# Optimization experiments

Measured on AMD Instinct MI355X. Metric: run time of the kernel, lower is better.

## Reference

```python
import jax, jax.numpy as jnp
import numpy as np

EPS = 1e-6
ROPE_BASE = 10000.0


def layer_norm(x, scale, bias):
    mu = jnp.mean(x, axis=-1, keepdims=True)
    var = jnp.mean(jnp.square(x - mu), axis=-1, keepdims=True)
    return (x - mu) * jax.lax.rsqrt(var + EPS) * scale + bias


def make_rope(head_dim, seq_len):
    half = head_dim // 2
    inv_freq = 1.0 / (ROPE_BASE ** (jnp.arange(half, dtype=jnp.float32) / half))
    freqs = jnp.outer(jnp.arange(seq_len, dtype=jnp.float32), inv_freq)  # (T, half)
    cos = jnp.concatenate([jnp.cos(freqs), jnp.cos(freqs)], axis=-1)[:, None, :]  # (T,1,Dh)
    sin = jnp.concatenate([jnp.sin(freqs), jnp.sin(freqs)], axis=-1)[:, None, :]

    def rotate_half(x):
        x1, x2 = x[..., :half], x[..., half:]
        return jnp.concatenate([-x2, x1], axis=-1)

    def apply(q, k):
        return q * cos + rotate_half(q) * sin, k * cos + rotate_half(k) * sin
    return apply


def mha(x, Wq, bq, Wk, bk, Wv, bv, Wo, bo, causal, rope):
    # x: (..., S, D) -> (..., S, D)
    q = jnp.einsum('...sd,dhk->...shk', x, Wq) + bq
    k = jnp.einsum('...sd,dhk->...shk', x, Wk) + bk
    v = jnp.einsum('...sd,dhk->...shk', x, Wv) + bv
    if rope is not None:
        q, k = rope(q, k)
    scale = 1.0 / np.sqrt(q.shape[-1]).astype(np.float32)
    logits = jnp.einsum('...thk,...shk->...hts', q, k) * scale
    if causal:
        S = q.shape[-3]
        mask = jnp.tril(jnp.ones((S, S), dtype=jnp.bool_))
        logits = jnp.where(mask, logits, jnp.finfo(logits.dtype).min)
    probs = jax.nn.softmax(logits, axis=-1)
    o = jnp.einsum('...hts,...shk->...thk', probs, v)
    return jnp.einsum('...thk,hkd->...td', o, Wo) + bo


def setup_inputs() -> dict:
    key = jax.random.key(0)
    B, T, M, D, H, Dh, F = 8, 128, 16, 1024, 16, 64, 4096
    ks = jax.random.split(key, 12)
    s = 0.02
    return {
        'x': jax.random.normal(ks[0], (B, T, M, D), jnp.float32),
        'ln1_scale': jnp.ones((D,), jnp.float32), 'ln1_bias': jnp.zeros((D,), jnp.float32),
        't_Wq': jax.random.normal(ks[1], (D, H, Dh), jnp.float32) * s,
        't_bq': jnp.zeros((H, Dh), jnp.float32),
        't_Wk': jax.random.normal(ks[2], (D, H, Dh), jnp.float32) * s,
        't_bk': jnp.zeros((H, Dh), jnp.float32),
        't_Wv': jax.random.normal(ks[3], (D, H, Dh), jnp.float32) * s,
        't_bv': jnp.zeros((H, Dh), jnp.float32),
        't_Wo': jax.random.normal(ks[4], (H, Dh, D), jnp.float32) * s,
        't_bo': jnp.zeros((D,), jnp.float32),
        'ln2_scale': jnp.ones((D,), jnp.float32), 'ln2_bias': jnp.zeros((D,), jnp.float32),
        'm_Wq': jax.random.normal(ks[5], (D, H, Dh), jnp.float32) * s,
        'm_bq': jnp.zeros((H, Dh), jnp.float32),
        'm_Wk': jax.random.normal(ks[6], (D, H, Dh), jnp.float32) * s,
        'm_bk': jnp.zeros((H, Dh), jnp.float32),
        'm_Wv': jax.random.normal(ks[7], (D, H, Dh), jnp.float32) * s,
        'm_bv': jnp.zeros((H, Dh), jnp.float32),
        'm_Wo': jax.random.normal(ks[8], (H, Dh, D), jnp.float32) * s,
        'm_bo': jnp.zeros((D,), jnp.float32),
        'ln3_scale': jnp.ones((D,), jnp.float32), 'ln3_bias': jnp.zeros((D,), jnp.float32),
        'mlp_W1': jax.random.normal(ks[9], (D, F), jnp.float32) * s,
        'mlp_b1': jnp.zeros((F,), jnp.float32),
        'mlp_W2': jax.random.normal(ks[10], (F, D), jnp.float32) * s,
        'mlp_b2': jnp.zeros((D,), jnp.float32),
    }


def reference(x, ln1_scale, ln1_bias, t_Wq, t_bq, t_Wk, t_bk, t_Wv, t_bv, t_Wo, t_bo,
              ln2_scale, ln2_bias, m_Wq, m_bq, m_Wk, m_bk, m_Wv, m_bv, m_Wo, m_bo,
              ln3_scale, ln3_bias, mlp_W1, mlp_b1, mlp_W2, mlp_b2):
    # x: (B, T, M, D)
    T = x.shape[1]
    Dh = t_Wq.shape[-1]
    rope = make_rope(Dh, T)
    # --- temporal axial attention (causal, RoPE), M folded into batch ---
    h = layer_norm(x, ln1_scale, ln1_bias)
    h = jnp.swapaxes(h, 1, 2)  # (B, M, T, D)
    a = mha(h, t_Wq, t_bq, t_Wk, t_bk, t_Wv, t_bv, t_Wo, t_bo, causal=True, rope=rope)
    x = x + jnp.swapaxes(a, 1, 2)
    # --- modality axial attention (bidirectional, no RoPE), T folded into batch ---
    h = layer_norm(x, ln2_scale, ln2_bias)  # (B, T, M, D), M is seq axis
    x = x + mha(h, m_Wq, m_bq, m_Wk, m_bk, m_Wv, m_bv, m_Wo, m_bo, causal=False, rope=None)
    # --- MLP ---
    h = layer_norm(x, ln3_scale, ln3_bias)
    h = jax.nn.gelu(jnp.einsum('...d,df->...f', h, mlp_W1) + mlp_b1)
    x = x + jnp.einsum('...f,fd->...d', h, mlp_W2) + mlp_b2
    return x
```

## Files before the change

kernel.cpp:

```cpp
#include <hip/hip_runtime.h>
#include <stdint.h>

typedef __attribute__((ext_vector_type(8))) __bf16 bf16x8;
typedef __attribute__((ext_vector_type(4))) float f32x4;

#define DEV static __device__ __forceinline__

DEV unsigned short f2bf(float f) {
    unsigned int u = __float_as_uint(f);
    u = (u + 0x7fffu + ((u >> 16) & 1u)) >> 16;
    return (unsigned short)u;
}
DEV float bf2f(unsigned short h) { return __uint_as_float((unsigned int)h << 16); }

DEV void async_ld16(const void* g, void* l) {
    __builtin_amdgcn_global_load_lds(
        (const __attribute__((address_space(1))) void*)g,
        (__attribute__((address_space(3))) void*)l, 16, 0, 0);
}

DEV f32x4 mfma16(bf16x8 a, bf16x8 b, f32x4 c) {
    return __builtin_amdgcn_mfma_f32_16x16x32_bf16(a, b, c, 0, 0, 0);
}

DEV float gelu_f(float v) {
    float u = 0.7978845608028654f * (v + 0.044715f * v * v * v);
    u = fminf(fmaxf(u, -9.f), 9.f);
    const float e = __expf(2.f * u);
    const float th = (e - 1.f) / (e + 1.f);
    return 0.5f * v * (1.0f + th);
}

__global__ __launch_bounds__(256) void wconv_kernel(
    const float* __restrict__ src, unsigned short* __restrict__ dst, int K, int N)
{
    __shared__ float tile[32][33];
    const int tx = threadIdx.x & 31;
    const int ty = threadIdx.x >> 5;
    const long nb = blockIdx.x;
    const long kb = blockIdx.y;
#pragma unroll
    for (int i = 0; i < 32; i += 8)
        tile[ty + i][tx] = src[(kb * 32 + ty + i) * N + nb * 32 + tx];
    __syncthreads();
#pragma unroll
    for (int i = 0; i < 32; i += 8)
        dst[(nb * 32 + ty + i) * K + kb * 32 + tx] = f2bf(tile[tx][ty + i]);
}

__global__ void pack_bias_kernel(const float* __restrict__ bq, const float* __restrict__ bk,
                                 const float* __restrict__ bv, float* __restrict__ o)
{
    int i = blockIdx.x * 256 + threadIdx.x;
    if (i < 1024) o[i] = bq[i];
    else if (i < 2048) o[i] = bk[i - 1024];
    else if (i < 3072) o[i] = bv[i - 2048];
}

__global__ __launch_bounds__(256) void ln_kernel(
    const float* __restrict__ x, const float* __restrict__ scale,
    const float* __restrict__ bias, unsigned short* __restrict__ out)
{
    const int lane = threadIdx.x & 63;
    const int wave = threadIdx.x >> 6;
    const long tok = (long)blockIdx.x * 4 + wave;
    const float* xp = x + tok * 1024;
    float4 v[4];
    float sum = 0.f, sq = 0.f;
#pragma unroll
    for (int i = 0; i < 4; ++i) {
        v[i] = ((const float4*)xp)[i * 64 + lane];
        sum += v[i].x + v[i].y + v[i].z + v[i].w;
        sq += v[i].x * v[i].x + v[i].y * v[i].y + v[i].z * v[i].z + v[i].w * v[i].w;
    }
#pragma unroll
    for (int off = 1; off < 64; off <<= 1) {
        sum += __shfl_xor(sum, off);
        sq  += __shfl_xor(sq, off);
    }
    const float mu = sum * (1.f / 1024.f);
    const float var = sq * (1.f / 1024.f) - mu * mu;
    const float rs = rsqrtf(var + 1e-6f);
#pragma unroll
    for (int i = 0; i < 4; ++i) {
        const float4 sc = ((const float4*)scale)[i * 64 + lane];
        const float4 bi = ((const float4*)bias)[i * 64 + lane];
        ushort4 o;
        o.x = f2bf((v[i].x - mu) * rs * sc.x + bi.x);
        o.y = f2bf((v[i].y - mu) * rs * sc.y + bi.y);
        o.z = f2bf((v[i].z - mu) * rs * sc.z + bi.z);
        o.w = f2bf((v[i].w - mu) * rs * sc.w + bi.w);
        *(ushort4*)&out[tok * 1024 + (i * 64 + lane) * 4] = o;
    }
}

template <int EPI, bool ROPE>
__global__ __launch_bounds__(256, 3) void gemm128_kernel(
    const unsigned short* __restrict__ A, const unsigned short* __restrict__ Bt,
    const float* __restrict__ bias, const float* __restrict__ resid,
    void* __restrict__ Cout, int M, int N, int K, int nbx)
{
    __shared__ __align__(16) unsigned short lds[2][2][4096];
    const int tid = threadIdx.x;
    const int lane = tid & 63;
    const int wave = tid >> 6;
    const int wr = wave >> 1;
    const int wc = wave & 1;
    const int lr = lane & 15;
    const int hi = lane >> 4;

    const int nwg = gridDim.x;
    const int cpx = nwg >> 3;
    int bid = blockIdx.x;
    bid = (bid & 7) * cpx + (bid >> 3);
    const int bx = bid % nbx, by = bid / nbx;
    const long row0 = (long)by * 128;
    const long col0 = (long)bx * 128;
    const int NT = K >> 5;

    const int r_ = tid >> 2;
    const int pc = tid & 3;
    const int sxr = (r_ >> 1) & 3;
    const unsigned short* gA0 = A + (row0 + r_) * (long)K + (pc ^ sxr) * 8;
    const unsigned short* gA1 = A + (row0 + r_ + 64) * (long)K + (pc ^ sxr) * 8;
    const unsigned short* gB0 = Bt + (col0 + r_) * (long)K + (pc ^ sxr) * 8;
    const unsigned short* gB1 = Bt + (col0 + r_ + 64) * (long)K + (pc ^ sxr) * 8;

    auto stage = [&](int buf, int kt) {
        const long ko = (long)kt * 32;
        async_ld16(gA0 + ko, &lds[buf][0][tid * 8]);
        async_ld16(gA1 + ko, &lds[buf][0][tid * 8 + 2048]);
        async_ld16(gB0 + ko, &lds[buf][1][tid * 8]);
        async_ld16(gB1 + ko, &lds[buf][1][tid * 8 + 2048]);
    };

    int aoff[4], boff[4];
#pragma unroll
    for (int m = 0; m < 4; ++m) {
        const int row = wr * 64 + m * 16 + lr;
        aoff[m] = row * 64 + ((hi ^ ((row >> 1) & 3)) << 4);
    }
#pragma unroll
    for (int n = 0; n < 4; ++n) {
        const int row = wc * 64 + n * 16 + lr;
        boff[n] = row * 64 + ((hi ^ ((row >> 1) & 3)) << 4);
    }

    f32x4 acc[4][4];
#pragma unroll
    for (int i = 0; i < 4; ++i)
#pragma unroll
        for (int j = 0; j < 4; ++j) acc[i][j] = f32x4{0.f, 0.f, 0.f, 0.f};

    stage(0, 0);

    for (int kt = 0; kt < NT; ++kt) {
        const int b = kt & 1;
        if (kt + 1 < NT) stage(b ^ 1, kt + 1);
        __builtin_amdgcn_sched_barrier(0);
        if (kt + 1 < NT) { asm volatile("s_waitcnt vmcnt(4)" ::: "memory"); }
        else             { asm volatile("s_waitcnt vmcnt(0)" ::: "memory"); }
        __builtin_amdgcn_sched_barrier(0);
        __builtin_amdgcn_s_barrier();
        __builtin_amdgcn_sched_barrier(0);

        const char* bA = (const char*)&lds[b][0][0];
        const char* bB = (const char*)&lds[b][1][0];
        bf16x8 a[4], bf[4];
#pragma unroll
        for (int n = 0; n < 4; ++n) bf[n] = *(const bf16x8*)(bB + boff[n]);
#pragma unroll
        for (int m = 0; m < 4; ++m) a[m] = *(const bf16x8*)(bA + aoff[m]);

        __builtin_amdgcn_s_setprio(1);
#pragma unroll
        for (int m = 0; m < 4; ++m)
#pragma unroll
            for (int n = 0; n < 4; ++n)
                acc[m][n] = mfma16(a[m], bf[n], acc[m][n]);
        __builtin_amdgcn_s_setprio(0);

        __builtin_amdgcn_sched_barrier(0);
        __builtin_amdgcn_s_barrier();
        __builtin_amdgcn_sched_barrier(0);
    }

    __syncthreads();

    float bcol[4];
#pragma unroll
    for (int n = 0; n < 4; ++n) bcol[n] = bias[col0 + wc * 64 + n * 16 + lr];

    if (EPI == 2) {
        float (*eF)[128] = (float (*)[128])&lds[0][0][0];
        float* co = (float*)Cout;
#pragma unroll
        for (int half = 0; half < 2; ++half) {
            if (wr == half) {
#pragma unroll
                for (int m = 0; m < 4; ++m)
#pragma unroll
                    for (int n = 0; n < 4; ++n)
#pragma unroll
                        for (int j = 0; j < 4; ++j)
                            eF[m * 16 + hi * 4 + j][wc * 64 + n * 16 + lr] =
                                acc[m][n][j] + bcol[n];
            }
            __syncthreads();
#pragma unroll
            for (int it = 0; it < 8; ++it) {
                const int idx = it * 256 + tid;
                const int row = idx >> 5;
                const int ch = (idx & 31) * 4;
                const long g = row0 + half * 64 + row;
                float4 v = *(const float4*)&eF[row][ch];
                const float4 rv = *(const float4*)&resid[g * N + col0 + ch];
                v.x += rv.x; v.y += rv.y; v.z += rv.z; v.w += rv.w;
                *(float4*)&co[g * N + col0 + ch] = v;
            }
            __syncthreads();
        }
    } else {
        unsigned short (*eT)[128] = (unsigned short (*)[128])&lds[0][0][0];
        unsigned short* co = (unsigned short*)Cout;
        const bool doRope = ROPE && (col0 + wc * 64) < 2048;
        if (doRope) {
#pragma unroll
            for (int m = 0; m < 4; ++m) {
                const float t_i = (float)(int)(((row0 + wr * 64 + m * 16) >> 4) & 127);
#pragma unroll
                for (int n = 0; n < 2; ++n) {
                    const float dd = (float)(n * 16 + lr);
                    const float inv = __expf(dd * -0.2878231366242557f);
                    float sn, cs;
                    __sincosf(t_i * inv, &sn, &cs);
#pragma unroll
                    for (int j = 0; j < 4; ++j) {
                        const float lo = acc[m][n][j] + bcol[n];
                        const float hv = acc[m][n + 2][j] + bcol[n + 2];
                        eT[wr * 64 + m * 16 + hi * 4 + j][wc * 64 + n * 16 + lr] = f2bf(lo * cs - hv * sn);
                        eT[wr * 64 + m * 16 + hi * 4 + j][wc * 64 + 32 + n * 16 + lr] = f2bf(hv * cs + lo * sn);
                    }
                }
            }
        } else {
#pragma unroll
            for (int m = 0; m < 4; ++m)
#pragma unroll
                for (int n = 0; n < 4; ++n)
#pragma unroll
                    for (int j = 0; j < 4; ++j) {
                        float v = acc[m][n][j] + bcol[n];
                        if (EPI == 1) v = gelu_f(v);
                        eT[wr * 64 + m * 16 + hi * 4 + j][wc * 64 + n * 16 + lr] = f2bf(v);
                    }
        }
        __syncthreads();
#pragma unroll
        for (int it = 0; it < 8; ++it) {
            const int idx = it * 256 + tid;
            const int row = idx >> 4;
            const int ch = (idx & 15) * 8;
            *(uint4*)&co[(row0 + row) * N + col0 + ch] = *(const uint4*)&eT[row][ch];
        }
    }
}

__global__ __launch_bounds__(256) void attn_temporal(
    const unsigned short* __restrict__ qkv, unsigned short* __restrict__ out)
{
    const int bid = blockIdx.x;
    const int h = bid & 15;
    const int mm = (bid >> 4) & 15;
    const int b = bid >> 8;
    const int tid = threadIdx.x;
    const int lane = tid & 63;
    const int wave = tid >> 6;
    const int lr = lane & 15;
    const int lk = (lane >> 4) * 8;
    const int r4 = (lane >> 4) * 4;

    __shared__ __align__(16) unsigned short smemA[128 * 136];
    __shared__ __align__(16) unsigned short smemV[64 * 136];
    unsigned short (*Ks)[72] = (unsigned short (*)[72])smemA;
    unsigned short (*Ps)[136] = (unsigned short (*)[136])smemA;
    unsigned short (*Vt)[136] = (unsigned short (*)[136])smemV;

    const long tokbase = (long)b * 2048 + mm;

#pragma unroll
    for (int i = 0; i < 4; ++i) {
        const int cc = tid + 256 * i;
        const int s = cc >> 3, part = cc & 7;
        const unsigned short* g = qkv + (tokbase + s * 16l) * 3072 + 1024 + h * 64 + part * 8;
        *(uint4*)&Ks[s][part * 8] = *(const uint4*)g;
    }
#pragma unroll
    for (int i = 0; i < 4; ++i) {
        const int cc = tid + 256 * i;
        const int s = cc >> 3, part = cc & 7;
        const unsigned short* g = qkv + (tokbase + s * 16l) * 3072 + 2048 + h * 64 + part * 8;
        union { uint4 u; unsigned short us[8]; } uu;
        uu.u = *(const uint4*)g;
#pragma unroll
        for (int j = 0; j < 8; ++j) Vt[part * 8 + j][s] = uu.us[j];
    }
    __syncthreads();

    bf16x8 qf[2][2];
#pragma unroll
    for (int rb = 0; rb < 2; ++rb)
#pragma unroll
        for (int ks = 0; ks < 2; ++ks) {
            const int t = wave * 32 + rb * 16 + lr;
            qf[rb][ks] = *(const bf16x8*)(qkv + (tokbase + t * 16l) * 3072 + h * 64 + ks * 32 + lk);
        }

    f32x4 sacc[2][8];
#pragma unroll
    for (int rb = 0; rb < 2; ++rb)
#pragma unroll
        for (int cb = 0; cb < 8; ++cb) sacc[rb][cb] = f32x4{0.f, 0.f, 0.f, 0.f};

#pragma unroll
    for (int cb = 0; cb < 8; ++cb)
#pragma unroll
        for (int ks = 0; ks < 2; ++ks) {
            const bf16x8 kf = *(const bf16x8*)&Ks[cb * 16 + lr][ks * 32 + lk];
            sacc[0][cb] = mfma16(qf[0][ks], kf, sacc[0][cb]);
            sacc[1][cb] = mfma16(qf[1][ks], kf, sacc[1][cb]);
        }

    float recip[2][4];
#pragma unroll
    for (int rb = 0; rb < 2; ++rb)
#pragma unroll
        for (int r = 0; r < 4; ++r) {
            const int trow = wave * 32 + rb * 16 + r4 + r;
            float mx = -1e30f;
#pragma unroll
            for (int cb = 0; cb < 8; ++cb) {
                const int s = cb * 16 + lr;
                const float v = (s <= trow) ? sacc[rb][cb][r] * 0.125f : -1e30f;
                sacc[rb][cb][r] = v;
                mx = fmaxf(mx, v);
            }
            mx = fmaxf(mx, __shfl_xor(mx, 1));
            mx = fmaxf(mx, __shfl_xor(mx, 2));
            mx = fmaxf(mx, __shfl_xor(mx, 4));
            mx = fmaxf(mx, __shfl_xor(mx, 8));
            float sum = 0.f;
#pragma unroll
            for (int cb = 0; cb < 8; ++cb) {
                const float e = __expf(sacc[rb][cb][r] - mx);
                sacc[rb][cb][r] = e;
                sum += e;
            }
            sum += __shfl_xor(sum, 1);
            sum += __shfl_xor(sum, 2);
            sum += __shfl_xor(sum, 4);
            sum += __shfl_xor(sum, 8);
            recip[rb][r] = 1.f / sum;
        }
    __syncthreads();

#pragma unroll
    for (int rb = 0; rb < 2; ++rb)
#pragma unroll
        for (int cb = 0; cb < 8; ++cb)
#pragma unroll
            for (int r = 0; r < 4; ++r)
                Ps[wave * 32 + rb * 16 + r4 + r][cb * 16 + lr] = f2bf(sacc[rb][cb][r]);
    __syncthreads();

    f32x4 oacc[2][4];
#pragma unroll
    for (int rb = 0; rb < 2; ++rb)
#pragma unroll
        for (int cb = 0; cb < 4; ++cb) oacc[rb][cb] = f32x4{0.f, 0.f, 0.f, 0.f};

#pragma unroll
    for (int ks = 0; ks < 4; ++ks) {
        bf16x8 pf[2];
        pf[0] = *(const bf16x8*)&Ps[wave * 32 + lr][ks * 32 + lk];
        pf[1] = *(const bf16x8*)&Ps[wave * 32 + 16 + lr][ks * 32 + lk];
#pragma unroll
        for (int cb = 0; cb < 4; ++cb) {
            const bf16x8 vf = *(const bf16x8*)&Vt[cb * 16 + lr][ks * 32 + lk];
            oacc[0][cb] = mfma16(pf[0], vf, oacc[0][cb]);
            oacc[1][cb] = mfma16(pf[1], vf, oacc[1][cb]);
        }
    }

#pragma unroll
    for (int rb = 0; rb < 2; ++rb)
#pragma unroll
        for (int cb = 0; cb < 4; ++cb)
#pragma unroll
            for (int r = 0; r < 4; ++r) {
                const int trow = wave * 32 + rb * 16 + r4 + r;
                out[(tokbase + trow * 16l) * 1024 + h * 64 + cb * 16 + lr] =
                    f2bf(oacc[rb][cb][r] * recip[rb][r]);
            }
}

__global__ __launch_bounds__(256) void attn_modality(
    const unsigned short* __restrict__ qkv, unsigned short* __restrict__ out)
{
    const int tid = threadIdx.x;
    const int lane = tid & 63;
    const int wave = tid >> 6;
    const int lr = lane & 15;
    const int lk = (lane >> 4) * 8;
    const int r4 = (lane >> 4) * 4;
    const long base = (long)blockIdx.x * 16;

    __shared__ __align__(16) unsigned short smem[4][64 * 40 + 16 * 40];
    unsigned short (*Vt)[40] = (unsigned short (*)[40]) & smem[wave][0];
    unsigned short (*Pl)[40] = (unsigned short (*)[40]) & smem[wave][64 * 40];

    for (int i = lane; i < 400; i += 64)
        *(uint4*)&smem[wave][i * 8] = make_uint4(0u, 0u, 0u, 0u);

    for (int hi = 0; hi < 4; ++hi) {
        const int h = wave * 4 + hi;
#pragma unroll
        for (int i = 0; i < 2; ++i) {
            const int cc = lane + 64 * i;
            const int s = cc >> 3, d0 = (cc & 7) * 8;
            union { uint4 u; unsigned short us[8]; } uu;
            uu.u = *(const uint4*)(qkv + (base + s) * 3072 + 2048 + h * 64 + d0);
#pragma unroll
            for (int j = 0; j < 8; ++j) Vt[d0 + j][s] = uu.us[j];
        }
        bf16x8 qf[2], kf[2];
#pragma unroll
        for (int ks = 0; ks < 2; ++ks) {
            qf[ks] = *(const bf16x8*)(qkv + (base + lr) * 3072 + h * 64 + ks * 32 + lk);
            kf[ks] = *(const bf16x8*)(qkv + (base + lr) * 3072 + 1024 + h * 64 + ks * 32 + lk);
        }
        f32x4 sv = f32x4{0.f, 0.f, 0.f, 0.f};
        sv = mfma16(qf[0], kf[0], sv);
        sv = mfma16(qf[1], kf[1], sv);

        float recip[4], pe[4];
#pragma unroll
        for (int r = 0; r < 4; ++r) {
            const float v = sv[r] * 0.125f;
            float mx = v;
            mx = fmaxf(mx, __shfl_xor(mx, 1));
            mx = fmaxf(mx, __shfl_xor(mx, 2));
            mx = fmaxf(mx, __shfl_xor(mx, 4));
            mx = fmaxf(mx, __shfl_xor(mx, 8));
            const float e = __expf(v - mx);
            float sum = e;
            sum += __shfl_xor(sum, 1);
            sum += __shfl_xor(sum, 2);
            sum += __shfl_xor(sum, 4);
            sum += __shfl_xor(sum, 8);
            recip[r] = 1.f / sum;
            pe[r] = e;
        }
#pragma unroll
        for (int r = 0; r < 4; ++r) Pl[r4 + r][lr] = f2bf(pe[r]);

        const bf16x8 pf = *(const bf16x8*)&Pl[lr][lk];
#pragma unroll
        for (int cb = 0; cb < 4; ++cb) {
            const bf16x8 vf = *(const bf16x8*)&Vt[cb * 16 + lr][lk];
            f32x4 o = f32x4{0.f, 0.f, 0.f, 0.f};
            o = mfma16(pf, vf, o);
#pragma unroll
            for (int r = 0; r < 4; ++r)
                out[(base + r4 + r) * 1024 + h * 64 + cb * 16 + lr] = f2bf(o[r] * recip[r]);
        }
    }
}

extern "C" void kernel_launch(void* const* d_in, const int* in_sizes, int n_in,
                              void* d_out, int out_size, void* d_ws, size_t ws_size,
                              hipStream_t stream)
{
    (void)in_sizes; (void)n_in; (void)out_size;
    const float* x    = (const float*)d_in[0];
    const float* ln1s = (const float*)d_in[1];
    const float* ln1b = (const float*)d_in[2];
    const float* tWq  = (const float*)d_in[3];
    const float* tbq  = (const float*)d_in[4];
    const float* tWk  = (const float*)d_in[5];
    const float* tbk  = (const float*)d_in[6];
    const float* tWv  = (const float*)d_in[7];
    const float* tbv  = (const float*)d_in[8];
    const float* tWo  = (const float*)d_in[9];
    const float* tbo  = (const float*)d_in[10];
    const float* ln2s = (const float*)d_in[11];
    const float* ln2b = (const float*)d_in[12];
    const float* mWq  = (const float*)d_in[13];
    const float* mbq  = (const float*)d_in[14];
    const float* mWk  = (const float*)d_in[15];
    const float* mbk  = (const float*)d_in[16];
    const float* mWv  = (const float*)d_in[17];
    const float* mbv  = (const float*)d_in[18];
    const float* mWo  = (const float*)d_in[19];
    const float* mbo  = (const float*)d_in[20];
    const float* ln3s = (const float*)d_in[21];
    const float* ln3b = (const float*)d_in[22];
    const float* W1   = (const float*)d_in[23];
    const float* b1   = (const float*)d_in[24];
    const float* W2   = (const float*)d_in[25];
    const float* b2   = (const float*)d_in[26];

    if (ws_size < 201351168ull) return;

    char* ws = (char*)d_ws;
    unsigned short* Wt_tqkv = (unsigned short*)(ws + 0);
    unsigned short* Wt_to   = (unsigned short*)(ws + 6291456);
    unsigned short* Wt_mqkv = (unsigned short*)(ws + 8388608);
    unsigned short* Wt_mo   = (unsigned short*)(ws + 14680064);
    unsigned short* Wt1     = (unsigned short*)(ws + 16777216);
    unsigned short* Wt2     = (unsigned short*)(ws + 25165824);
    float* bias_t           = (float*)(ws + 33554432);
    float* bias_m           = (float*)(ws + 33566720);
    unsigned short* act     = (unsigned short*)(ws + 33579008);
    unsigned short* qkv     = (unsigned short*)(ws + 67133440);
    unsigned short* hidden  = qkv;
    float* xout = (float*)d_out;

    dim3 blk(256);

    wconv_kernel<<<dim3(32, 32), blk, 0, stream>>>(tWq, Wt_tqkv, 1024, 1024);
    wconv_kernel<<<dim3(32, 32), blk, 0, stream>>>(tWk, Wt_tqkv + 1024 * 1024, 1024, 1024);
    wconv_kernel<<<dim3(32, 32), blk, 0, stream>>>(tWv, Wt_tqkv + 2048 * 1024, 1024, 1024);
    wconv_kernel<<<dim3(32, 32), blk, 0, stream>>>(tWo, Wt_to, 1024, 1024);
    wconv_kernel<<<dim3(32, 32), blk, 0, stream>>>(mWq, Wt_mqkv, 1024, 1024);
    wconv_kernel<<<dim3(32, 32), blk, 0, stream>>>(mWk, Wt_mqkv + 1024 * 1024, 1024, 1024);
    wconv_kernel<<<dim3(32, 32), blk, 0, stream>>>(mWv, Wt_mqkv + 2048 * 1024, 1024, 1024);
    wconv_kernel<<<dim3(32, 32), blk, 0, stream>>>(mWo, Wt_mo, 1024, 1024);
    wconv_kernel<<<dim3(128, 32), blk, 0, stream>>>(W1, Wt1, 1024, 4096);
    wconv_kernel<<<dim3(32, 128), blk, 0, stream>>>(W2, Wt2, 4096, 1024);
    pack_bias_kernel<<<12, blk, 0, stream>>>(tbq, tbk, tbv, bias_t);
    pack_bias_kernel<<<12, blk, 0, stream>>>(mbq, mbk, mbv, bias_m);

    ln_kernel<<<4096, blk, 0, stream>>>(x, ln1s, ln1b, act);
    gemm128_kernel<0, true><<<3072, blk, 0, stream>>>(act, Wt_tqkv, bias_t, nullptr, qkv, 16384, 3072, 1024, 24);
    attn_temporal<<<2048, blk, 0, stream>>>(qkv, act);
    gemm128_kernel<2, false><<<1024, blk, 0, stream>>>(act, Wt_to, tbo, x, xout, 16384, 1024, 1024, 8);
    ln_kernel<<<4096, blk, 0, stream>>>(xout, ln2s, ln2b, act);
    gemm128_kernel<0, false><<<3072, blk, 0, stream>>>(act, Wt_mqkv, bias_m, nullptr, qkv, 16384, 3072, 1024, 24);
    attn_modality<<<1024, blk, 0, stream>>>(qkv, act);
    gemm128_kernel<2, false><<<1024, blk, 0, stream>>>(act, Wt_mo, mbo, xout, xout, 16384, 1024, 1024, 8);
    ln_kernel<<<4096, blk, 0, stream>>>(xout, ln3s, ln3b, act);
    gemm128_kernel<1, false><<<4096, blk, 0, stream>>>(act, Wt1, b1, nullptr, hidden, 16384, 4096, 1024, 32);
    gemm128_kernel<2, false><<<1024, blk, 0, stream>>>(hidden, Wt2, b2, xout, xout, 16384, 1024, 4096, 8);
}
```

Baseline: 861.1 us.

## Enlarge GEMM tile to 256x128 with 8-wave 512-thread blocks

Changes the GEMM from 128x128 tiles with 4 waves to 256x128 tiles with 8 waves (512 threads), so each B tile loaded into LDS is shared by twice as many rows. Global loads per k-step per thread drop from 4 to 3, and the epilogues are restaged in quarters or halves through the same LDS buffer. The goal is less global and LDS traffic for B per output element and fewer blocks. The cost is more epilogue barriers, a larger LDS footprint per block, and fewer blocks in the grid.

```diff
diff --git a/kernel.cpp b/kernel.cpp
--- a/kernel.cpp
+++ b/kernel.cpp
@@ -95,17 +95,17 @@
 }
 
 template <int EPI, bool ROPE>
-__global__ __launch_bounds__(256, 3) void gemm128_kernel(
+__global__ __launch_bounds__(512, 4) void gemm_kernel(
     const unsigned short* __restrict__ A, const unsigned short* __restrict__ Bt,
     const float* __restrict__ bias, const float* __restrict__ resid,
     void* __restrict__ Cout, int M, int N, int K, int nbx)
 {
-    __shared__ __align__(16) unsigned short lds[2][2][4096];
+    __shared__ __align__(16) unsigned short lds[2][12288];
     const int tid = threadIdx.x;
     const int lane = tid & 63;
     const int wave = tid >> 6;
-    const int wr = wave >> 1;
-    const int wc = wave & 1;
+    const int wm = wave >> 1;
+    const int wn = wave & 1;
     const int lr = lane & 15;
     const int hi = lane >> 4;
 
@@ -114,36 +114,33 @@
     int bid = blockIdx.x;
     bid = (bid & 7) * cpx + (bid >> 3);
     const int bx = bid % nbx, by = bid / nbx;
-    const long row0 = (long)by * 128;
+    const long row0 = (long)by * 256;
     const long col0 = (long)bx * 128;
     const int NT = K >> 5;
 
     const int r_ = tid >> 2;
-    const int pc = tid & 3;
-    const int sxr = (r_ >> 1) & 3;
-    const unsigned short* gA0 = A + (row0 + r_) * (long)K + (pc ^ sxr) * 8;
-    const unsigned short* gA1 = A + (row0 + r_ + 64) * (long)K + (pc ^ sxr) * 8;
-    const unsigned short* gB0 = Bt + (col0 + r_) * (long)K + (pc ^ sxr) * 8;
-    const unsigned short* gB1 = Bt + (col0 + r_ + 64) * (long)K + (pc ^ sxr) * 8;
+    const int gch = ((tid & 3) ^ ((tid >> 3) & 3)) * 8;
+    const unsigned short* srcA0 = A + (row0 + r_) * (long)K + gch;
+    const unsigned short* srcA1 = A + (row0 + 128 + r_) * (long)K + gch;
+    const unsigned short* srcB  = Bt + (col0 + r_) * (long)K + gch;
 
     auto stage = [&](int buf, int kt) {
         const long ko = (long)kt * 32;
-        async_ld16(gA0 + ko, &lds[buf][0][tid * 8]);
-        async_ld16(gA1 + ko, &lds[buf][0][tid * 8 + 2048]);
-        async_ld16(gB0 + ko, &lds[buf][1][tid * 8]);
-        async_ld16(gB1 + ko, &lds[buf][1][tid * 8 + 2048]);
+        async_ld16(srcA0 + ko, &lds[buf][tid * 8]);
+        async_ld16(srcA1 + ko, &lds[buf][4096 + tid * 8]);
+        async_ld16(srcB  + ko, &lds[buf][8192 + tid * 8]);
     };
 
     int aoff[4], boff[4];
 #pragma unroll
     for (int m = 0; m < 4; ++m) {
-        const int row = wr * 64 + m * 16 + lr;
+        const int row = wm * 64 + m * 16 + lr;
         aoff[m] = row * 64 + ((hi ^ ((row >> 1) & 3)) << 4);
     }
 #pragma unroll
     for (int n = 0; n < 4; ++n) {
-        const int row = wc * 64 + n * 16 + lr;
-        boff[n] = row * 64 + ((hi ^ ((row >> 1) & 3)) << 4);
+        const int row = wn * 64 + n * 16 + lr;
+        boff[n] = 16384 + row * 64 + ((hi ^ ((row >> 1) & 3)) << 4);
     }
 
     f32x4 acc[4][4];
@@ -158,26 +155,25 @@
         const int b = kt & 1;
         if (kt + 1 < NT) stage(b ^ 1, kt + 1);
         __builtin_amdgcn_sched_barrier(0);
-        if (kt + 1 < NT) { asm volatile("s_waitcnt vmcnt(4)" ::: "memory"); }
+        if (kt + 1 < NT) { asm volatile("s_waitcnt vmcnt(3)" ::: "memory"); }
         else             { asm volatile("s_waitcnt vmcnt(0)" ::: "memory"); }
         __builtin_amdgcn_sched_barrier(0);
         __builtin_amdgcn_s_barrier();
         __builtin_amdgcn_sched_barrier(0);
 
-        const char* bA = (const char*)&lds[b][0][0];
-        const char* bB = (const char*)&lds[b][1][0];
-        bf16x8 a[4], bf[4];
-#pragma unroll
-        for (int n = 0; n < 4; ++n) bf[n] = *(const bf16x8*)(bB + boff[n]);
-#pragma unroll
-        for (int m = 0; m < 4; ++m) a[m] = *(const bf16x8*)(bA + aoff[m]);
+        const char* base = (const char*)&lds[b][0];
+        bf16x8 a[4], bfr[4];
+#pragma unroll
+        for (int n = 0; n < 4; ++n) bfr[n] = *(const bf16x8*)(base + boff[n]);
+#pragma unroll
+        for (int m = 0; m < 4; ++m) a[m] = *(const bf16x8*)(base + aoff[m]);
 
         __builtin_amdgcn_s_setprio(1);
 #pragma unroll
         for (int m = 0; m < 4; ++m)
 #pragma unroll
             for (int n = 0; n < 4; ++n)
-                acc[m][n] = mfma16(a[m], bf[n], acc[m][n]);
+                acc[m][n] = mfma16(a[m], bfr[n], acc[m][n]);
         __builtin_amdgcn_s_setprio(0);
 
         __builtin_amdgcn_sched_barrier(0);
@@ -189,30 +185,30 @@
 
     float bcol[4];
 #pragma unroll
-    for (int n = 0; n < 4; ++n) bcol[n] = bias[col0 + wc * 64 + n * 16 + lr];
+    for (int n = 0; n < 4; ++n) bcol[n] = bias[col0 + wn * 64 + n * 16 + lr];
 
     if (EPI == 2) {
-        float (*eF)[128] = (float (*)[128])&lds[0][0][0];
+        float (*eF)[128] = (float (*)[128])&lds[0][0];
         float* co = (float*)Cout;
 #pragma unroll
-        for (int half = 0; half < 2; ++half) {
-            if (wr == half) {
+        for (int q = 0; q < 4; ++q) {
+            if (wm == q) {
 #pragma unroll
                 for (int m = 0; m < 4; ++m)
 #pragma unroll
                     for (int n = 0; n < 4; ++n)
 #pragma unroll
                         for (int j = 0; j < 4; ++j)
-                            eF[m * 16 + hi * 4 + j][wc * 64 + n * 16 + lr] =
+                            eF[m * 16 + hi * 4 + j][wn * 64 + n * 16 + lr] =
                                 acc[m][n][j] + bcol[n];
             }
             __syncthreads();
 #pragma unroll
-            for (int it = 0; it < 8; ++it) {
-                const int idx = it * 256 + tid;
+            for (int it = 0; it < 4; ++it) {
+                const int idx = it * 512 + tid;
                 const int row = idx >> 5;
                 const int ch = (idx & 31) * 4;
-                const long g = row0 + half * 64 + row;
+                const long g = row0 + q * 64 + row;
                 float4 v = *(const float4*)&eF[row][ch];
                 const float4 rv = *(const float4*)&resid[g * N + col0 + ch];
                 v.x += rv.x; v.y += rv.y; v.z += rv.z; v.w += rv.w;
@@ -221,47 +217,54 @@
             __syncthreads();
         }
     } else {
-        unsigned short (*eT)[128] = (unsigned short (*)[128])&lds[0][0][0];
+        unsigned short (*eT)[128] = (unsigned short (*)[128])&lds[0][0];
         unsigned short* co = (unsigned short*)Cout;
-        const bool doRope = ROPE && (col0 + wc * 64) < 2048;
-        if (doRope) {
-#pragma unroll
-            for (int m = 0; m < 4; ++m) {
-                const float t_i = (float)(int)(((row0 + wr * 64 + m * 16) >> 4) & 127);
-#pragma unroll
-                for (int n = 0; n < 2; ++n) {
-                    const float dd = (float)(n * 16 + lr);
-                    const float inv = __expf(dd * -0.2878231366242557f);
-                    float sn, cs;
-                    __sincosf(t_i * inv, &sn, &cs);
-#pragma unroll
-                    for (int j = 0; j < 4; ++j) {
-                        const float lo = acc[m][n][j] + bcol[n];
-                        const float hv = acc[m][n + 2][j] + bcol[n + 2];
-                        eT[wr * 64 + m * 16 + hi * 4 + j][wc * 64 + n * 16 + lr] = f2bf(lo * cs - hv * sn);
-                        eT[wr * 64 + m * 16 + hi * 4 + j][wc * 64 + 32 + n * 16 + lr] = f2bf(hv * cs + lo * sn);
+        const bool doRope = ROPE && (col0 + wn * 64) < 2048;
+#pragma unroll
+        for (int h2 = 0; h2 < 2; ++h2) {
+            if ((wm >> 1) == h2) {
+                const int r64 = (wm & 1) * 64;
+                if (doRope) {
+#pragma unroll
+                    for (int m = 0; m < 4; ++m) {
+                        const float t_i = (float)(int)(((row0 + wm * 64 + m * 16) >> 4) & 127);
+#pragma unroll
+                        for (int n = 0; n < 2; ++n) {
+                            const float dd = (float)(n * 16 + lr);
+                            const float inv = __expf(dd * -0.2878231366242557f);
+                            float sn, cs;
+                            __sincosf(t_i * inv, &sn, &cs);
+#pragma unroll
+                            for (int j = 0; j < 4; ++j) {
+                                const float lo = acc[m][n][j] + bcol[n];
+                                const float hv = acc[m][n + 2][j] + bcol[n + 2];
+                                eT[r64 + m * 16 + hi * 4 + j][wn * 64 + n * 16 + lr] = f2bf(lo * cs - hv * sn);
+                                eT[r64 + m * 16 + hi * 4 + j][wn * 64 + 32 + n * 16 + lr] = f2bf(hv * cs + lo * sn);
+                            }
+                        }
                     }
+                } else {
+#pragma unroll
+                    for (int m = 0; m < 4; ++m)
+#pragma unroll
+                        for (int n = 0; n < 4; ++n)
+#pragma unroll
+                            for (int j = 0; j < 4; ++j) {
+                                float v = acc[m][n][j] + bcol[n];
+                                if (EPI == 1) v = gelu_f(v);
+                                eT[r64 + m * 16 + hi * 4 + j][wn * 64 + n * 16 + lr] = f2bf(v);
+                            }
                 }
             }
-        } else {
-#pragma unroll
-            for (int m = 0; m < 4; ++m)
-#pragma unroll
-                for (int n = 0; n < 4; ++n)
-#pragma unroll
-                    for (int j = 0; j < 4; ++j) {
-                        float v = acc[m][n][j] + bcol[n];
-                        if (EPI == 1) v = gelu_f(v);
-                        eT[wr * 64 + m * 16 + hi * 4 + j][wc * 64 + n * 16 + lr] = f2bf(v);
-                    }
-        }
-        __syncthreads();
-#pragma unroll
-        for (int it = 0; it < 8; ++it) {
-            const int idx = it * 256 + tid;
-            const int row = idx >> 4;
-            const int ch = (idx & 15) * 8;
-            *(uint4*)&co[(row0 + row) * N + col0 + ch] = *(const uint4*)&eT[row][ch];
+            __syncthreads();
+#pragma unroll
+            for (int it = 0; it < 4; ++it) {
+                const int idx = it * 512 + tid;
+                const int row = idx >> 4;
+                const int ch = (idx & 15) * 8;
+                *(uint4*)&co[(row0 + h2 * 128 + row) * N + col0 + ch] = *(const uint4*)&eT[row][ch];
+            }
+            __syncthreads();
         }
     }
 }
@@ -527,6 +530,7 @@
     float* xout = (float*)d_out;
 
     dim3 blk(256);
+    dim3 blk5(512);
 
     wconv_kernel<<<dim3(32, 32), blk, 0, stream>>>(tWq, Wt_tqkv, 1024, 1024);
     wconv_kernel<<<dim3(32, 32), blk, 0, stream>>>(tWk, Wt_tqkv + 1024 * 1024, 1024, 1024);
@@ -542,14 +546,14 @@
     pack_bias_kernel<<<12, blk, 0, stream>>>(mbq, mbk, mbv, bias_m);
 
     ln_kernel<<<4096, blk, 0, stream>>>(x, ln1s, ln1b, act);
-    gemm128_kernel<0, true><<<3072, blk, 0, stream>>>(act, Wt_tqkv, bias_t, nullptr, qkv, 16384, 3072, 1024, 24);
+    gemm_kernel<0, true><<<1536, blk5, 0, stream>>>(act, Wt_tqkv, bias_t, nullptr, qkv, 16384, 3072, 1024, 24);
     attn_temporal<<<2048, blk, 0, stream>>>(qkv, act);
-    gemm128_kernel<2, false><<<1024, blk, 0, stream>>>(act, Wt_to, tbo, x, xout, 16384, 1024, 1024, 8);
+    gemm_kernel<2, false><<<512, blk5, 0, stream>>>(act, Wt_to, tbo, x, xout, 16384, 1024, 1024, 8);
     ln_kernel<<<4096, blk, 0, stream>>>(xout, ln2s, ln2b, act);
-    gemm128_kernel<0, false><<<3072, blk, 0, stream>>>(act, Wt_mqkv, bias_m, nullptr, qkv, 16384, 3072, 1024, 24);
+    gemm_kernel<0, false><<<1536, blk5, 0, stream>>>(act, Wt_mqkv, bias_m, nullptr, qkv, 16384, 3072, 1024, 24);
     attn_modality<<<1024, blk, 0, stream>>>(qkv, act);
-    gemm128_kernel<2, false><<<1024, blk, 0, stream>>>(act, Wt_mo, mbo, xout, xout, 16384, 1024, 1024, 8);
+    gemm_kernel<2, false><<<512, blk5, 0, stream>>>(act, Wt_mo, mbo, xout, xout, 16384, 1024, 1024, 8);
     ln_kernel<<<4096, blk, 0, stream>>>(xout, ln3s, ln3b, act);
-    gemm128_kernel<1, false><<<4096, blk, 0, stream>>>(act, Wt1, b1, nullptr, hidden, 16384, 4096, 1024, 32);
-    gemm128_kernel<2, false><<<1024, blk, 0, stream>>>(hidden, Wt2, b2, xout, xout, 16384, 1024, 4096, 8);
-}
+    gemm_kernel<1, false><<<2048, blk5, 0, stream>>>(act, Wt1, b1, nullptr, hidden, 16384, 4096, 1024, 32);
+    gemm_kernel<2, false><<<512, blk5, 0, stream>>>(hidden, Wt2, b2, xout, xout, 16384, 1024, 4096, 8);
+}
```

Result: faster. 793.2 us (-7.9%).
